# Kernel tuning notes

Measured on AMD Instinct MI355X. Metric: run time of the kernel, lower is better.

## Reference

```python
import jax, jax.numpy as jnp
import numpy as np

N_NODES = 50000
N_EDGES = 800000
N_GRAPHS = 2500
IN_DIM = 128
HID = 64
HEADS = 2
NEG_SLOPE = 0.2


def _gat_layer(x, W, att_src, att_dst, bias, src, dst, n):
    # W: [F_in, H*C], att_*: [H, C], bias: [C]
    h = (x @ W).reshape(n, HEADS, HID)            # [N,H,C]
    a_src = jnp.sum(h * att_src[None], axis=-1)   # [N,H]
    a_dst = jnp.sum(h * att_dst[None], axis=-1)   # [N,H]
    e = jax.nn.leaky_relu(a_src[src] + a_dst[dst], NEG_SLOPE)  # [E,H]
    # segment softmax over destination neighborhoods
    m = jax.ops.segment_max(e, dst, num_segments=n)            # [N,H]
    m = jnp.where(jnp.isfinite(m), m, 0.0)
    ex = jnp.exp(e - m[dst])
    s = jax.ops.segment_sum(ex, dst, num_segments=n)           # [N,H]
    alpha = ex / jnp.maximum(s[dst], 1e-16)                    # [E,H]
    msg = h[src] * alpha[:, :, None]                           # [E,H,C]
    out = jax.ops.segment_sum(msg, dst, num_segments=n)        # [N,H,C]
    return out.mean(axis=1) + bias                             # concat=False -> head mean


def _with_self_loops(edge_index, n):
    loop = jnp.arange(n, dtype=edge_index.dtype)
    src = jnp.concatenate([edge_index[0], loop])
    dst = jnp.concatenate([edge_index[1], loop])
    return src, dst


def setup_inputs() -> dict:
    key = jax.random.key(0)
    ks = jax.random.split(key, 16)
    x = jax.random.normal(ks[0], (N_NODES, IN_DIM), dtype=jnp.float32)
    edge_index = jax.random.randint(ks[1], (2, N_EDGES), 0, N_NODES, dtype=jnp.int32)
    batch = jnp.sort(jax.random.randint(ks[2], (N_NODES,), 0, N_GRAPHS, dtype=jnp.int32))

    def glorot(k, shape):
        fan = shape[0] + shape[-1]
        return jax.random.normal(k, shape, dtype=jnp.float32) * np.sqrt(2.0 / fan)

    inp = {"x": x, "edge_index": edge_index, "batch": batch}
    dims = [IN_DIM, HID, HID]
    for i in range(3):
        inp[f"W{i+1}"] = glorot(ks[3 + 4 * i], (dims[i], HEADS * HID))
        inp[f"att_src{i+1}"] = glorot(ks[4 + 4 * i], (HEADS, HID))
        inp[f"att_dst{i+1}"] = glorot(ks[5 + 4 * i], (HEADS, HID))
        inp[f"b{i+1}"] = jnp.zeros((HID,), dtype=jnp.float32)
    inp["lin_w"] = glorot(ks[15], (HID, 1))
    inp["lin_b"] = jnp.zeros((1,), dtype=jnp.float32)
    return inp


def reference(x, W1, att_src1, att_dst1, b1, W2, att_src2, att_dst2, b2,
              W3, att_src3, att_dst3, b3, lin_w, lin_b, edge_index, batch):
    n = x.shape[0]
    src, dst = _with_self_loops(edge_index, n)
    h = jax.nn.relu(_gat_layer(x, W1, att_src1, att_dst1, b1, src, dst, n))
    h = jax.nn.relu(_gat_layer(h, W2, att_src2, att_dst2, b2, src, dst, n))
    h = jax.nn.relu(_gat_layer(h, W3, att_src3, att_dst3, b3, src, dst, n))
    # global mean pool over graphs
    sums = jax.ops.segment_sum(h, batch, num_segments=N_GRAPHS)          # [G,C]
    cnt = jax.ops.segment_sum(jnp.ones((n,), h.dtype), batch, num_segments=N_GRAPHS)
    pooled = sums / jnp.maximum(cnt, 1.0)[:, None]
    return pooled @ lin_w + lin_b                                        # [G,1]
```

## Files before the change

### kernel.cpp

```cpp
#include <hip/hip_runtime.h>
#include <hip/hip_fp16.h>
#include <math.h>


__device__ __forceinline__ float lrelu(float v) { return v > 0.f ? v : 0.2f * v; }

__device__ __forceinline__ float wave_max(float v) {
  for (int off = 32; off; off >>= 1) v = fmaxf(v, __shfl_xor(v, off, 64));
  return v;
}
__device__ __forceinline__ float half_sum(float v) {
  for (int off = 16; off; off >>= 1) v += __shfl_xor(v, off, 64);
  return v;
}
__device__ __forceinline__ float half_max(float v) {
  for (int off = 16; off; off >>= 1) v = fmaxf(v, __shfl_xor(v, off, 64));
  return v;
}

typedef _Float16 f16x8 __attribute__((ext_vector_type(8)));
typedef float f32x4 __attribute__((ext_vector_type(4)));

__device__ __forceinline__ int colperm(int l, int ks) {
  return l == 0 ? ks : (((ks & 3) << 4) | ((ks >> 3) << 1) | ((ks >> 2) & 1));
}

__global__ void count_rank_prep(const int* __restrict__ ei, int* __restrict__ deg,
                                int* __restrict__ rank, int e, int eb,
                                const float* __restrict__ W1, const float* __restrict__ as1,
                                const float* __restrict__ ad1,
                                const float* __restrict__ W2, const float* __restrict__ as2,
                                const float* __restrict__ ad2,
                                const float* __restrict__ W3, const float* __restrict__ as3,
                                const float* __restrict__ ad3,
                                __half* __restrict__ WT1, __half* __restrict__ WT2,
                                __half* __restrict__ WT3) {
  int bx = blockIdx.x;
  if (bx < eb) {
    int j0 = bx * 1024 + threadIdx.x;
#pragma unroll
    for (int k = 0; k < 4; ++k) {
      int j = j0 + k * 256;
      if (j < e) rank[j] = atomicAdd(&deg[ei[e + j]], 1);
    }
    return;
  }
  int pb = bx - eb;
  int l = pb >> 3, part = pb & 7;
  const float* W = l == 0 ? W1 : (l == 1 ? W2 : W3);
  const float* as = l == 0 ? as1 : (l == 1 ? as2 : as3);
  const float* ad = l == 0 ? ad1 : (l == 1 ? ad2 : ad3);
  __half* WT = l == 0 ? WT1 : (l == 1 ? WT2 : WT3);
  const int shk = l == 0 ? 7 : 6;
  const int K = 1 << shk;
  for (int idx = part * 256 + threadIdx.x; idx < 144 * K; idx += 2048) {
    int row = idx >> shk;
    int ks = idx & (K - 1);
    int kt = colperm(l, ks);
    float val;
    if (row < 128) {
      val = W[kt * 128 + row];
    } else if (row < 132) {
      int j = row - 128;
      const float* att = (j < 2 ? as : ad) + (j & 1) * 64;
      const float* wr = W + kt * 128 + (j & 1) * 64;
      float acc = 0.f;
#pragma unroll
      for (int c = 0; c < 64; ++c) acc = fmaf(wr[c], att[c], acc);
      val = acc;
    } else {
      val = 0.f;
    }
    WT[idx] = __float2half(val);
  }
}

__global__ void scan_blocks(const int* __restrict__ deg, int* __restrict__ row_ptr,
                            int* __restrict__ btot, int n) {
  __shared__ int sm[256];
  int i = blockIdx.x * 256 + threadIdx.x;
  int v = (i < n) ? deg[i] : 0;
  sm[threadIdx.x] = v;
  __syncthreads();
  for (int off = 1; off < 256; off <<= 1) {
    int t = (threadIdx.x >= off) ? sm[threadIdx.x - off] : 0;
    __syncthreads();
    sm[threadIdx.x] += t;
    __syncthreads();
  }
  if (i < n) row_ptr[i] = sm[threadIdx.x] - v;
  if (threadIdx.x == 255) btot[blockIdx.x] = sm[255];
}

__global__ void scan_totals(int* __restrict__ btot, int nb) {
  __shared__ int sm[256];
  int v = (threadIdx.x < nb) ? btot[threadIdx.x] : 0;
  sm[threadIdx.x] = v;
  __syncthreads();
  for (int off = 1; off < 256; off <<= 1) {
    int t = (threadIdx.x >= off) ? sm[threadIdx.x - off] : 0;
    __syncthreads();
    sm[threadIdx.x] += t;
    __syncthreads();
  }
  if (threadIdx.x < nb) btot[threadIdx.x] = sm[threadIdx.x] - v;
}

__global__ void scan_add(int* __restrict__ row_ptr, int* __restrict__ csr,
                         const int* __restrict__ btot, int n, int total) {
  int i = blockIdx.x * 256 + threadIdx.x;
  if (i < n) {
    int v = row_ptr[i] + btot[blockIdx.x] + i;
    row_ptr[i] = v;
    csr[v] = i;
  }
  if (i == 0) row_ptr[n] = total;
}

__global__ void place_kernel(const int* __restrict__ ei, const int* __restrict__ rank,
                             const int* __restrict__ row_ptr, int* __restrict__ csr,
                             int e) {
  int j0 = blockIdx.x * 1024 + threadIdx.x;
#pragma unroll
  for (int k = 0; k < 4; ++k) {
    int j = j0 + k * 256;
    if (j < e) {
      int d = ei[e + j];
      csr[row_ptr[d] + 1 + rank[j]] = ei[j];
    }
  }
}

template <int K, bool F16IN>
__global__ __launch_bounds__(256) void gemm_mfma(const void* __restrict__ Xv,
                                                 const __half* __restrict__ WT,
                                                 __half* __restrict__ H16,
                                                 float* __restrict__ a_src,
                                                 float* __restrict__ a_dst, int N) {
  constexpr int KP = K + 8;
  extern __shared__ __half smem[];
  __half* Al = smem;
  __half* Wl = smem + 64 * KP;
  int tid = threadIdx.x;
  int row0 = blockIdx.x * 64;

  if constexpr (F16IN) {
    const __half* X = (const __half*)Xv;
    constexpr int CH = K / 8;
    for (int idx = tid; idx < 64 * CH; idx += 256) {
      int r = idx / CH, ch = idx % CH;
      int gr = row0 + r; if (gr >= N) gr = N - 1;
      *(uint4*)&Al[r * KP + ch * 8] = *(const uint4*)(X + (size_t)gr * K + ch * 8);
    }
  } else {
    const float* X = (const float*)Xv;
    constexpr int CH4 = K / 4;
    for (int idx = tid; idx < 64 * CH4; idx += 256) {
      int r = idx / CH4, ch = idx % CH4;
      int gr = row0 + r; if (gr >= N) gr = N - 1;
      float4 v = *(const float4*)(X + (size_t)gr * K + ch * 4);
      union { __half2 h2[2]; uint2 u; } t;
      t.h2[0] = __floats2half2_rn(v.x, v.y);
      t.h2[1] = __floats2half2_rn(v.z, v.w);
      *(uint2*)&Al[r * KP + ch * 4] = t.u;
    }
  }
  constexpr int CHW = K / 8;
  for (int idx = tid; idx < 144 * CHW; idx += 256) {
    int r = idx / CHW, ch = idx % CHW;
    *(uint4*)&Wl[r * KP + ch * 8] = *(const uint4*)(WT + r * K + ch * 8);
  }
  __syncthreads();

  int lane = tid & 63;
  int wv = tid >> 6;
  int q = lane & 15;
  int kg = lane >> 4;

  f32x4 acc[9] = {};
  const __half* ap = &Al[(wv * 16 + q) * KP + kg * 8];
  const __half* wp = &Wl[q * KP + kg * 8];
#pragma unroll
  for (int ks = 0; ks < K / 32; ++ks) {
    f16x8 a = *(const f16x8*)(ap + ks * 32);
#pragma unroll
    for (int n = 0; n < 9; ++n) {
      f16x8 b = *(const f16x8*)(wp + n * 16 * KP + ks * 32);
      acc[n] = __builtin_amdgcn_mfma_f32_16x16x32_f16(a, b, acc[n], 0, 0, 0);
    }
  }

#pragma unroll
  for (int reg = 0; reg < 4; ++reg) {
    int r = row0 + wv * 16 + kg * 4 + reg;
    if (r < N) {
      union { __half2 h2[2]; uint2 u; } s0, s1;
      s0.h2[0] = __floats2half2_rn(acc[0][reg], acc[1][reg]);
      s0.h2[1] = __floats2half2_rn(acc[2][reg], acc[3][reg]);
      s1.h2[0] = __floats2half2_rn(acc[4][reg], acc[5][reg]);
      s1.h2[1] = __floats2half2_rn(acc[6][reg], acc[7][reg]);
      *(uint2*)(H16 + (size_t)r * 128 + q * 4) = s0.u;
      *(uint2*)(H16 + (size_t)r * 128 + 64 + q * 4) = s1.u;
      float av = acc[8][reg];
      if (q < 2) a_src[r * 2 + q] = av;
      else if (q < 4) a_dst[r * 2 + q - 2] = av;
    }
  }
}

__device__ __forceinline__ void ld_grp8(const __half* __restrict__ H16, int half_,
                                        int c8, int headsel, int sub, int s,
                                        float p0, float p1, int g,
                                        uint4* h, float* q) {
#pragma unroll
  for (int k = 0; k < 4; ++k) {
    int idx = half_ + g * 8 + k * 2 + sub;
    int st = __shfl(s, idx, 64);
    float q0 = __shfl(p0, idx, 64);
    float q1 = __shfl(p1, idx, 64);
    q[k] = headsel ? q1 : q0;
    h[k] = *(const uint4*)(H16 + (size_t)st * 128 + c8);
  }
}
__device__ __forceinline__ void fma_grp8(const uint4* h, const float* q,
                                         float* acc) {
#pragma unroll
  for (int k = 0; k < 4; ++k) {
    union { uint u; __half2 h2; } a, b, c, d;
    a.u = h[k].x; b.u = h[k].y; c.u = h[k].z; d.u = h[k].w;
    float2 f0 = __half22float2(a.h2);
    float2 f1 = __half22float2(b.h2);
    float2 f2 = __half22float2(c.h2);
    float2 f3 = __half22float2(d.h2);
    acc[0] = fmaf(f0.x, q[k], acc[0]);
    acc[1] = fmaf(f0.y, q[k], acc[1]);
    acc[2] = fmaf(f1.x, q[k], acc[2]);
    acc[3] = fmaf(f1.y, q[k], acc[3]);
    acc[4] = fmaf(f2.x, q[k], acc[4]);
    acc[5] = fmaf(f2.y, q[k], acc[5]);
    acc[6] = fmaf(f3.x, q[k], acc[6]);
    acc[7] = fmaf(f3.y, q[k], acc[7]);
  }
}
__device__ __forceinline__ void gather_pipe8(const __half* __restrict__ H16, int half_,
                                             int c8, int headsel, int sub, int s,
                                             float p0, float p1, int maxcnt,
                                             float* acc) {
  int groups = (maxcnt + 7) >> 3;
  uint4 ha[4], hb[4];
  float qa[4], qb[4];
  ld_grp8(H16, half_, c8, headsel, sub, s, p0, p1, 0, ha, qa);
  int g = 1;
  for (; g + 1 < groups; g += 2) {
    ld_grp8(H16, half_, c8, headsel, sub, s, p0, p1, g, hb, qb);
    fma_grp8(ha, qa, acc);
    ld_grp8(H16, half_, c8, headsel, sub, s, p0, p1, g + 1, ha, qa);
    fma_grp8(hb, qb, acc);
  }
  if (g < groups) {
    ld_grp8(H16, half_, c8, headsel, sub, s, p0, p1, g, hb, qb);
    fma_grp8(ha, qa, acc);
    fma_grp8(hb, qb, acc);
  } else {
    fma_grp8(ha, qa, acc);
  }
}

template <int POOL>
__global__ __launch_bounds__(256) void aggregate_fused(
    const __half* __restrict__ H16, const float* __restrict__ a_src,
    const float* __restrict__ a_dst, const float* __restrict__ bias,
    const int* __restrict__ row_ptr, const int* __restrict__ csr,
    __half* __restrict__ out, const float* __restrict__ lw,
    float* __restrict__ pvn, int N) {
  int lane = threadIdx.x & 63;
  int half_ = lane & 32;
  int l32 = lane & 31;
  int dst = blockIdx.x * 8 + ((threadIdx.x >> 6) << 1) + (half_ >> 5);
  bool live = dst < N;
  int beg = live ? row_ptr[dst] : 0;
  int end = live ? row_ptr[dst + 1] : 0;
  int cnt = end - beg;
  float2 ad = live ? ((const float2*)a_dst)[dst] : make_float2(0.f, 0.f);
  int sub = l32 >> 4;
  int m = l32 & 15;
  int c8 = m * 8;
  int headsel = m >> 3;
  float acc[8] = {};
  float inv0, inv1;

  int maxcnt = (int)wave_max((float)cnt);
  if (maxcnt < 1) maxcnt = 1;

  if (maxcnt <= 32) {
    int j = beg + l32;
    bool valid = l32 < cnt;
    int s = valid ? csr[j] : 0;
    float2 as = ((const float2*)a_src)[s];
    float e0 = valid ? lrelu(as.x + ad.x) : -1e30f;
    float e1 = valid ? lrelu(as.y + ad.y) : -1e30f;
    float m0 = half_max(e0);
    float m1 = half_max(e1);
    float p0 = __expf(e0 - m0);
    float p1 = __expf(e1 - m1);
    inv0 = 1.f / fmaxf(half_sum(valid ? p0 : 0.f), 1e-16f);
    inv1 = 1.f / fmaxf(half_sum(valid ? p1 : 0.f), 1e-16f);
    gather_pipe8(H16, half_, c8, headsel, sub, s, p0, p1, maxcnt, acc);
  } else {
    float m0 = -1e30f, m1 = -1e30f, s0 = 0.f, s1 = 0.f;
    for (int base = 0; base < maxcnt; base += 32) {
      int j = beg + base + l32;
      bool valid = (base + l32) < cnt;
      int s = valid ? csr[j] : 0;
      float2 as = ((const float2*)a_src)[s];
      float e0 = valid ? lrelu(as.x + ad.x) : -1e30f;
      float e1 = valid ? lrelu(as.y + ad.y) : -1e30f;
      float nm0 = fmaxf(m0, half_max(e0));
      float nm1 = fmaxf(m1, half_max(e1));
      s0 = s0 * __expf(m0 - nm0) + half_sum(valid ? __expf(e0 - nm0) : 0.f);
      s1 = s1 * __expf(m1 - nm1) + half_sum(valid ? __expf(e1 - nm1) : 0.f);
      m0 = nm0; m1 = nm1;
    }
    inv0 = 1.f / fmaxf(s0, 1e-16f);
    inv1 = 1.f / fmaxf(s1, 1e-16f);
    for (int base = 0; base < maxcnt; base += 32) {
      int j = beg + base + l32;
      bool valid = (base + l32) < cnt;
      int s = valid ? csr[j] : 0;
      float2 as = ((const float2*)a_src)[s];
      float e0 = valid ? lrelu(as.x + ad.x) : -1e30f;
      float e1 = valid ? lrelu(as.y + ad.y) : -1e30f;
      float p0 = __expf(e0 - m0);
      float p1 = __expf(e1 - m1);
      int rem = maxcnt - base;
      if (rem > 32) rem = 32;
      gather_pipe8(H16, half_, c8, headsel, sub, s, p0, p1, rem, acc);
    }
  }

#pragma unroll
  for (int j = 0; j < 8; ++j) acc[j] += __shfl_xor(acc[j], 16, 64);

  float il = headsel ? inv1 : inv0;
  float v[8], w[8];
#pragma unroll
  for (int j = 0; j < 8; ++j) v[j] = acc[j] * il;
#pragma unroll
  for (int j = 0; j < 8; ++j) w[j] = __shfl_xor(v[j], 8, 64);

  if (m < 8 && sub == 0 && live) {
    int cb = m << 1;
    float r[8];
#pragma unroll
    for (int j = 0; j < 8; ++j) {
      int c = ((j & 3) << 4) + cb + (j >> 2);
      r[j] = fmaxf(0.5f * (v[j] + w[j]) + bias[c], 0.f);
    }
    if (POOL) {
      float pv = 0.f;
#pragma unroll
      for (int j = 0; j < 8; ++j) {
        int c = ((j & 3) << 4) + cb + (j >> 2);
        pv = fmaf(r[j], lw[c], pv);
      }
      pv += __shfl_xor(pv, 1, 64);
      pv += __shfl_xor(pv, 2, 64);
      pv += __shfl_xor(pv, 4, 64);
      if (m == 0) pvn[dst] = pv;
    } else {
      union { __half2 h2[4]; uint4 u; } pk;
      pk.h2[0] = __floats2half2_rn(r[0], r[1]);
      pk.h2[1] = __floats2half2_rn(r[2], r[3]);
      pk.h2[2] = __floats2half2_rn(r[4], r[5]);
      pk.h2[3] = __floats2half2_rn(r[6], r[7]);
      *(uint4*)(out + (size_t)dst * 64 + m * 8) = pk.u;
    }
  }
}

__device__ __forceinline__ int lower_bound(const int* __restrict__ a, int n, int key) {
  int lo = 0, hi = n;
  while (lo < hi) {
    int mid = (lo + hi) >> 1;
    if (a[mid] < key) lo = mid + 1; else hi = mid;
  }
  return lo;
}

__global__ void finalize_kernel(const float* __restrict__ pvn,
                                const int* __restrict__ batch,
                                const float* __restrict__ lb,
                                float* __restrict__ out, int N, int G) {
  int g = blockIdx.x * blockDim.x + threadIdx.x;
  if (g >= G) return;
  int lo = lower_bound(batch, N, g);
  int hi = lower_bound(batch, N, g + 1);
  float s = 0.f;
  for (int i = lo; i < hi; ++i) s += pvn[i];
  out[g] = s / fmaxf((float)(hi - lo), 1.f) + lb[0];
}

extern "C" void kernel_launch(void* const* d_in, const int* in_sizes, int n_in,
                              void* d_out, int out_size, void* d_ws, size_t ws_size,
                              hipStream_t stream) {
  const float* x   = (const float*)d_in[0];
  const int* ei    = (const int*)d_in[1];
  const int* batch = (const int*)d_in[2];
  const float* W1  = (const float*)d_in[3];
  const float* as1 = (const float*)d_in[4];
  const float* ad1 = (const float*)d_in[5];
  const float* b1  = (const float*)d_in[6];
  const float* W2  = (const float*)d_in[7];
  const float* as2 = (const float*)d_in[8];
  const float* ad2 = (const float*)d_in[9];
  const float* b2  = (const float*)d_in[10];
  const float* W3  = (const float*)d_in[11];
  const float* as3 = (const float*)d_in[12];
  const float* ad3 = (const float*)d_in[13];
  const float* b3  = (const float*)d_in[14];
  const float* lw  = (const float*)d_in[15];
  const float* lb  = (const float*)d_in[16];
  float* out = (float*)d_out;

  const int N = in_sizes[0] / 128;
  const int E = in_sizes[1] / 2;
  const int ET = N + E;
  const int G = out_size;
  const int NB = (N + 255) / 256;
  const int EB = (E + 1023) / 1024;

  char* p = (char*)d_ws;
  auto take = [&](size_t bytes) {
    char* r = p;
    p += (bytes + 255) & ~(size_t)255;
    return r;
  };
  int* deg      = (int*)take((size_t)N * 4);
  int* row_ptr  = (int*)take((size_t)(N + 1) * 4);
  int* rank     = (int*)take((size_t)E * 4);
  int* btot     = (int*)take((size_t)NB * 4);
  int* csr      = (int*)take((size_t)ET * 4);
  __half* H16   = (__half*)take((size_t)N * 128 * 2);
  float* a_src  = (float*)take((size_t)N * 2 * 4);
  float* a_dst  = (float*)take((size_t)N * 2 * 4);
  __half* bufA  = (__half*)take((size_t)N * 64 * 2);
  __half* bufB  = (__half*)take((size_t)N * 64 * 2);
  float* pvn    = (float*)take((size_t)N * 4);
  __half* WT1   = (__half*)take((size_t)144 * 128 * 2);
  __half* WT2   = (__half*)take((size_t)144 * 64 * 2);
  __half* WT3   = (__half*)take((size_t)144 * 64 * 2);
  (void)ws_size; (void)n_in;

  hipMemsetAsync(deg, 0, (size_t)N * 4, stream);
  count_rank_prep<<<EB + 24, 256, 0, stream>>>(ei, deg, rank, E, EB,
                                               W1, as1, ad1, W2, as2, ad2,
                                               W3, as3, ad3, WT1, WT2, WT3);
  scan_blocks<<<NB, 256, 0, stream>>>(deg, row_ptr, btot, N);
  scan_totals<<<1, 256, 0, stream>>>(btot, NB);
  scan_add<<<NB, 256, 0, stream>>>(row_ptr, csr, btot, N, ET);
  place_kernel<<<EB, 256, 0, stream>>>(ei, rank, row_ptr, csr, E);

  const int gblk = (N + 63) / 64;
  const int ablk = (N + 7) / 8;
  constexpr int LDS1 = (64 + 144) * (128 + 8) * 2;
  constexpr int LDS2 = (64 + 144) * (64 + 8) * 2;

  gemm_mfma<128, false><<<gblk, 256, LDS1, stream>>>(x, WT1, H16, a_src, a_dst, N);
  aggregate_fused<0><<<ablk, 256, 0, stream>>>(H16, a_src, a_dst, b1, row_ptr, csr,
                                               bufA, lw, pvn, N);
  gemm_mfma<64, true><<<gblk, 256, LDS2, stream>>>(bufA, WT2, H16, a_src, a_dst, N);
  aggregate_fused<0><<<ablk, 256, 0, stream>>>(H16, a_src, a_dst, b2, row_ptr, csr,
                                               bufB, lw, pvn, N);
  gemm_mfma<64, true><<<gblk, 256, LDS2, stream>>>(bufB, WT3, H16, a_src, a_dst, N);
  aggregate_fused<1><<<ablk, 256, 0, stream>>>(H16, a_src, a_dst, b3, row_ptr, csr,
                                               bufA, lw, pvn, N);

  finalize_kernel<<<(G + 255) / 256, 256, 0, stream>>>(pvn, batch, lb, out, N, G);
}
```

Baseline: 308.8 us.

## Fuse aggregation with next layer GEMM and merge scan kernels

The per-layer aggregation now writes its 8 output rows into LDS, and the same block runs the next layer's projection with MFMA instructions. It also computes the attention logits a_src and a_dst there, which removes the separate gemm kernels for layers 2 and 3 and the fp16 round-trip of the intermediate activations. Ping-pong H and attention buffers are added because the fused kernel reads one layer's features while writing the next. The scan_totals and scan_add kernels are merged so that each block re-scans the block totals itself, saving one launch. In exchange, each 8-row block re-reads the weight tile from global memory and runs MFMAs on only 8 of 16 rows.

```diff
diff --git a/kernel.cpp b/kernel.cpp
--- a/kernel.cpp
+++ b/kernel.cpp
@@ -92,7 +92,8 @@
   if (threadIdx.x == 255) btot[blockIdx.x] = sm[255];
 }
 
-__global__ void scan_totals(int* __restrict__ btot, int nb) {
+__global__ void scan_add2(int* __restrict__ row_ptr, int* __restrict__ csr,
+                          const int* __restrict__ btot, int n, int total, int nb) {
   __shared__ int sm[256];
   int v = (threadIdx.x < nb) ? btot[threadIdx.x] : 0;
   sm[threadIdx.x] = v;
@@ -103,16 +104,12 @@
     sm[threadIdx.x] += t;
     __syncthreads();
   }
-  if (threadIdx.x < nb) btot[threadIdx.x] = sm[threadIdx.x] - v;
-}
-
-__global__ void scan_add(int* __restrict__ row_ptr, int* __restrict__ csr,
-                         const int* __restrict__ btot, int n, int total) {
+  int base = sm[blockIdx.x] - btot[blockIdx.x];
   int i = blockIdx.x * 256 + threadIdx.x;
   if (i < n) {
-    int v = row_ptr[i] + btot[blockIdx.x] + i;
-    row_ptr[i] = v;
-    csr[v] = i;
+    int v2 = row_ptr[i] + base + i;
+    row_ptr[i] = v2;
+    csr[v2] = i;
   }
   if (i == 0) row_ptr[n] = total;
 }
@@ -266,17 +263,13 @@
   }
 }
 
-template <int POOL>
-__global__ __launch_bounds__(256) void aggregate_fused(
+__device__ __forceinline__ bool agg_body(
     const __half* __restrict__ H16, const float* __restrict__ a_src,
-    const float* __restrict__ a_dst, const float* __restrict__ bias,
-    const int* __restrict__ row_ptr, const int* __restrict__ csr,
-    __half* __restrict__ out, const float* __restrict__ lw,
-    float* __restrict__ pvn, int N) {
+    const float* __restrict__ a_dst, const int* __restrict__ row_ptr,
+    const int* __restrict__ csr, int dst, int N, float* v, float* w, int* m_out) {
   int lane = threadIdx.x & 63;
   int half_ = lane & 32;
   int l32 = lane & 31;
-  int dst = blockIdx.x * 8 + ((threadIdx.x >> 6) << 1) + (half_ >> 5);
   bool live = dst < N;
   int beg = live ? row_ptr[dst] : 0;
   int end = live ? row_ptr[dst + 1] : 0;
@@ -342,13 +335,33 @@
   for (int j = 0; j < 8; ++j) acc[j] += __shfl_xor(acc[j], 16, 64);
 
   float il = headsel ? inv1 : inv0;
+#pragma unroll
+  for (int j = 0; j < 8; ++j) v[j] = acc[j] * il;
+#pragma unroll
+  for (int j = 0; j < 8; ++j) w[j] = __shfl_xor(v[j], 8, 64);
+
+  *m_out = m;
+  return (m < 8) && (sub == 0) && live;
+}
+
+__global__ __launch_bounds__(256) void agg_gemm(
+    const __half* __restrict__ Hin, const float* __restrict__ a_src,
+    const float* __restrict__ a_dst, const float* __restrict__ bias,
+    const int* __restrict__ row_ptr, const int* __restrict__ csr,
+    const __half* __restrict__ WT, __half* __restrict__ Hout,
+    float* __restrict__ as_out, float* __restrict__ ad_out, int N) {
+  constexpr int KP = 72;
+  __shared__ __half Als[16 * KP];
+  int lane = threadIdx.x & 63;
+  int wv = threadIdx.x >> 6;
+  int r_loc = (wv << 1) + ((lane & 32) >> 5);
+  int dst = blockIdx.x * 8 + r_loc;
+
   float v[8], w[8];
-#pragma unroll
-  for (int j = 0; j < 8; ++j) v[j] = acc[j] * il;
-#pragma unroll
-  for (int j = 0; j < 8; ++j) w[j] = __shfl_xor(v[j], 8, 64);
-
-  if (m < 8 && sub == 0 && live) {
+  int m;
+  bool writer = agg_body(Hin, a_src, a_dst, row_ptr, csr, dst, N, v, w, &m);
+
+  if (writer) {
     int cb = m << 1;
     float r[8];
 #pragma unroll
@@ -356,26 +369,86 @@
       int c = ((j & 3) << 4) + cb + (j >> 2);
       r[j] = fmaxf(0.5f * (v[j] + w[j]) + bias[c], 0.f);
     }
-    if (POOL) {
-      float pv = 0.f;
-#pragma unroll
-      for (int j = 0; j < 8; ++j) {
-        int c = ((j & 3) << 4) + cb + (j >> 2);
-        pv = fmaf(r[j], lw[c], pv);
+    union { __half2 h2[4]; uint4 u; } pk;
+    pk.h2[0] = __floats2half2_rn(r[0], r[1]);
+    pk.h2[1] = __floats2half2_rn(r[2], r[3]);
+    pk.h2[2] = __floats2half2_rn(r[4], r[5]);
+    pk.h2[3] = __floats2half2_rn(r[6], r[7]);
+    *(uint4*)&Als[r_loc * KP + m * 8] = pk.u;
+  }
+  __syncthreads();
+
+  int q = lane & 15;
+  int kg = lane >> 4;
+  int row0 = blockIdx.x * 8;
+  int n0 = 2 * wv, n1 = 2 * wv + 1;
+  f32x4 acc0 = {}, acc1 = {}, accA = {};
+  const __half* ap = &Als[q * KP + kg * 8];
+#pragma unroll
+  for (int ks = 0; ks < 2; ++ks) {
+    f16x8 a = *(const f16x8*)(ap + ks * 32);
+    f16x8 b0 = *(const f16x8*)(WT + (size_t)(16 * n0 + q) * 64 + kg * 8 + ks * 32);
+    f16x8 b1 = *(const f16x8*)(WT + (size_t)(16 * n1 + q) * 64 + kg * 8 + ks * 32);
+    acc0 = __builtin_amdgcn_mfma_f32_16x16x32_f16(a, b0, acc0, 0, 0, 0);
+    acc1 = __builtin_amdgcn_mfma_f32_16x16x32_f16(a, b1, acc1, 0, 0, 0);
+    if (wv == 0) {
+      f16x8 ba = *(const f16x8*)(WT + (size_t)(128 + q) * 64 + kg * 8 + ks * 32);
+      accA = __builtin_amdgcn_mfma_f32_16x16x32_f16(a, ba, accA, 0, 0, 0);
+    }
+  }
+
+  if (kg < 2) {
+    int h = wv >> 1, p = wv & 1;
+#pragma unroll
+    for (int reg = 0; reg < 4; ++reg) {
+      int r = row0 + kg * 4 + reg;
+      if (r < N) {
+        __half2 hv = __floats2half2_rn(acc0[reg], acc1[reg]);
+        *(__half2*)(Hout + (size_t)r * 128 + h * 64 + q * 4 + 2 * p) = hv;
       }
-      pv += __shfl_xor(pv, 1, 64);
-      pv += __shfl_xor(pv, 2, 64);
-      pv += __shfl_xor(pv, 4, 64);
-      if (m == 0) pvn[dst] = pv;
-    } else {
-      union { __half2 h2[4]; uint4 u; } pk;
-      pk.h2[0] = __floats2half2_rn(r[0], r[1]);
-      pk.h2[1] = __floats2half2_rn(r[2], r[3]);
-      pk.h2[2] = __floats2half2_rn(r[4], r[5]);
-      pk.h2[3] = __floats2half2_rn(r[6], r[7]);
-      *(uint4*)(out + (size_t)dst * 64 + m * 8) = pk.u;
-    }
-  }
+    }
+    if (wv == 0) {
+#pragma unroll
+      for (int reg = 0; reg < 4; ++reg) {
+        int r = row0 + kg * 4 + reg;
+        if (r < N) {
+          float av = accA[reg];
+          if (q < 2) as_out[r * 2 + q] = av;
+          else if (q < 4) ad_out[r * 2 + q - 2] = av;
+        }
+      }
+    }
+  }
+}
+
+__global__ __launch_bounds__(256) void aggregate_pool(
+    const __half* __restrict__ H16, const float* __restrict__ a_src,
+    const float* __restrict__ a_dst, const float* __restrict__ bias,
+    const int* __restrict__ row_ptr, const int* __restrict__ csr,
+    const float* __restrict__ lw, float* __restrict__ pvn, int N) {
+  int lane = threadIdx.x & 63;
+  int wv = threadIdx.x >> 6;
+  int dst = blockIdx.x * 8 + (wv << 1) + ((lane & 32) >> 5);
+
+  float v[8], w[8];
+  int m;
+  bool writer = agg_body(H16, a_src, a_dst, row_ptr, csr, dst, N, v, w, &m);
+
+  int l32 = lane & 31;
+  float pv = 0.f;
+  if (writer) {
+    int cb = m << 1;
+#pragma unroll
+    for (int j = 0; j < 8; ++j) {
+      int c = ((j & 3) << 4) + cb + (j >> 2);
+      float r = fmaxf(0.5f * (v[j] + w[j]) + bias[c], 0.f);
+      pv = fmaf(r, lw[c], pv);
+    }
+  }
+  pv += __shfl_xor(pv, 1, 64);
+  pv += __shfl_xor(pv, 2, 64);
+  pv += __shfl_xor(pv, 4, 64);
+  if (writer && (l32 & 7) == 0 && m == 0) pvn[dst] = pv;
 }
 
 __device__ __forceinline__ int lower_bound(const int* __restrict__ a, int n, int key) {
@@ -440,11 +513,12 @@
   int* rank     = (int*)take((size_t)E * 4);
   int* btot     = (int*)take((size_t)NB * 4);
   int* csr      = (int*)take((size_t)ET * 4);
-  __half* H16   = (__half*)take((size_t)N * 128 * 2);
-  float* a_src  = (float*)take((size_t)N * 2 * 4);
-  float* a_dst  = (float*)take((size_t)N * 2 * 4);
-  __half* bufA  = (__half*)take((size_t)N * 64 * 2);
-  __half* bufB  = (__half*)take((size_t)N * 64 * 2);
+  __half* H16A  = (__half*)take((size_t)N * 128 * 2);
+  __half* H16B  = (__half*)take((size_t)N * 128 * 2);
+  float* asA    = (float*)take((size_t)N * 2 * 4);
+  float* adA    = (float*)take((size_t)N * 2 * 4);
+  float* asB    = (float*)take((size_t)N * 2 * 4);
+  float* adB    = (float*)take((size_t)N * 2 * 4);
   float* pvn    = (float*)take((size_t)N * 4);
   __half* WT1   = (__half*)take((size_t)144 * 128 * 2);
   __half* WT2   = (__half*)take((size_t)144 * 64 * 2);
@@ -456,24 +530,20 @@
                                                W1, as1, ad1, W2, as2, ad2,
                                                W3, as3, ad3, WT1, WT2, WT3);
   scan_blocks<<<NB, 256, 0, stream>>>(deg, row_ptr, btot, N);
-  scan_totals<<<1, 256, 0, stream>>>(btot, NB);
-  scan_add<<<NB, 256, 0, stream>>>(row_ptr, csr, btot, N, ET);
+  scan_add2<<<NB, 256, 0, stream>>>(row_ptr, csr, btot, N, ET, NB);
   place_kernel<<<EB, 256, 0, stream>>>(ei, rank, row_ptr, csr, E);
 
   const int gblk = (N + 63) / 64;
   const int ablk = (N + 7) / 8;
   constexpr int LDS1 = (64 + 144) * (128 + 8) * 2;
-  constexpr int LDS2 = (64 + 144) * (64 + 8) * 2;
-
-  gemm_mfma<128, false><<<gblk, 256, LDS1, stream>>>(x, WT1, H16, a_src, a_dst, N);
-  aggregate_fused<0><<<ablk, 256, 0, stream>>>(H16, a_src, a_dst, b1, row_ptr, csr,
-                                               bufA, lw, pvn, N);
-  gemm_mfma<64, true><<<gblk, 256, LDS2, stream>>>(bufA, WT2, H16, a_src, a_dst, N);
-  aggregate_fused<0><<<ablk, 256, 0, stream>>>(H16, a_src, a_dst, b2, row_ptr, csr,
-                                               bufB, lw, pvn, N);
-  gemm_mfma<64, true><<<gblk, 256, LDS2, stream>>>(bufB, WT3, H16, a_src, a_dst, N);
-  aggregate_fused<1><<<ablk, 256, 0, stream>>>(H16, a_src, a_dst, b3, row_ptr, csr,
-                                               bufA, lw, pvn, N);
+
+  gemm_mfma<128, false><<<gblk, 256, LDS1, stream>>>(x, WT1, H16A, asA, adA, N);
+  agg_gemm<<<ablk, 256, 0, stream>>>(H16A, asA, adA, b1, row_ptr, csr, WT2,
+                                     H16B, asB, adB, N);
+  agg_gemm<<<ablk, 256, 0, stream>>>(H16B, asB, adB, b2, row_ptr, csr, WT3,
+                                     H16A, asA, adA, N);
+  aggregate_pool<<<ablk, 256, 0, stream>>>(H16A, asA, adA, b3, row_ptr, csr,
+                                           lw, pvn, N);
 
   finalize_kernel<<<(G + 255) / 256, 256, 0, stream>>>(pvn, batch, lb, out, N, G);
 }
```

Result: slower. 322.6 us (+4.5%).
